# Kernel tuning notes

Hardware: AMD Instinct MI355X
Metric: run time of the kernel (lower is better)

The kernel has to match this reference:

```python
import jax, jax.numpy as jnp
import numpy as np

H = 16          # num_heads
D = 1024        # in_features
NH = D // H     # per-head dim
EPS = 1e-5


def _ln(x, g, b):
    m = jnp.mean(x, axis=-1, keepdims=True)
    v = jnp.mean((x - m) ** 2, axis=-1, keepdims=True)
    return (x - m) / jnp.sqrt(v + EPS) * g + b


def _mha(q, k, v, Wq, bq, Wk, bk, Wv, bv, causal):
    # q: [Tq,B,D], k/v: [Tk,B,D]
    Tq, B, _ = q.shape
    Tk = k.shape[0]
    qh = (q @ Wq + bq).reshape(Tq, B, H, NH)
    kh = (k @ Wk + bk).reshape(Tk, B, H, NH)
    vh = (v @ Wv + bv).reshape(Tk, B, H, NH)
    scale = 1.0 / np.float32(np.sqrt(NH))
    logits = jnp.einsum('qbhd,kbhd->bhqk', qh, kh) * scale  # [B,H,Tq,Tk]
    if causal:
        mask = jnp.tril(jnp.ones((Tq, Tk), dtype=bool))
        logits = jnp.where(mask, logits, -jnp.inf)  # softmax over prefix [0..t]
    w = jax.nn.softmax(logits, axis=-1)
    out = jnp.einsum('bhqk,kbhd->qbhd', w, vh).reshape(Tq, B, D)
    return out


def setup_inputs() -> dict:
    key = jax.random.key(0)
    ks = jax.random.split(key, 12)
    s = 0.02
    T, B = 1024, 8
    inp = {
        'encoder_input': jax.random.normal(ks[0], (T, B, D), jnp.float32),
        'decoder_input': jax.random.normal(ks[1], (T, B, D), jnp.float32),
        # self-attention projections
        'Wq1': jax.random.normal(ks[2], (D, D), jnp.float32) * s,
        'bq1': jnp.zeros((D,), jnp.float32),
        'Wk1': jax.random.normal(ks[3], (D, D), jnp.float32) * s,
        'bk1': jnp.zeros((D,), jnp.float32),
        'Wv1': jax.random.normal(ks[4], (D, D), jnp.float32) * s,
        'bv1': jnp.zeros((D,), jnp.float32),
        # cross-attention projections
        'Wq2': jax.random.normal(ks[5], (D, D), jnp.float32) * s,
        'bq2': jnp.zeros((D,), jnp.float32),
        'Wk2': jax.random.normal(ks[6], (D, D), jnp.float32) * s,
        'bk2': jnp.zeros((D,), jnp.float32),
        'Wv2': jax.random.normal(ks[7], (D, D), jnp.float32) * s,
        'bv2': jnp.zeros((D,), jnp.float32),
        # position-wise linear
        'Wl': jax.random.normal(ks[8], (D, D), jnp.float32) * s,
        'bl': jnp.zeros((D,), jnp.float32),
        # layernorms
        'g1': jnp.ones((D,), jnp.float32), 'be1': jnp.zeros((D,), jnp.float32),
        'g2': jnp.ones((D,), jnp.float32), 'be2': jnp.zeros((D,), jnp.float32),
        'g3': jnp.ones((D,), jnp.float32), 'be3': jnp.zeros((D,), jnp.float32),
    }
    return inp


def reference(encoder_input, decoder_input,
              Wq1, bq1, Wk1, bk1, Wv1, bv1,
              Wq2, bq2, Wk2, bk2, Wv2, bv2,
              Wl, bl, g1, be1, g2, be2, g3, be3):
    # causal self-attention (prefix [:t+1] per step == causal mask)
    x = _mha(decoder_input, decoder_input, decoder_input,
             Wq1, bq1, Wk1, bk1, Wv1, bv1, causal=True)
    x = _ln(x + decoder_input, g1, be1)
    # cross-attention over full encoder input
    y = _mha(x, encoder_input, encoder_input,
             Wq2, bq2, Wk2, bk2, Wv2, bv2, causal=False)
    y = _ln(y + x, g2, be2)
    # position-wise linear (no activation in source) + residual + LN
    z = y @ Wl + bl
    out = _ln(z + y, g3, be3)
    return out
```

## Files before the change

### kernel.cpp

```cpp
#include <hip/hip_runtime.h>
#include <hip/hip_bf16.h>

typedef __bf16 bf16x8 __attribute__((ext_vector_type(8)));
typedef float f32x4 __attribute__((ext_vector_type(4)));

#define MFMA16(A, B, C) __builtin_amdgcn_mfma_f32_16x16x32_bf16(A, B, C, 0, 0, 0)

#define GLDS(gp, lp)                                                              \
    __builtin_amdgcn_global_load_lds(                                             \
        (const __attribute__((address_space(1))) void*)(gp),                      \
        (__attribute__((address_space(3))) void*)(lp), 16, 0, 0)

struct PtrW { const float* p[7]; };
__global__ __launch_bounds__(256) void wt_transpose(PtrW W, __hip_bfloat16* __restrict__ Wt) {
    const float* __restrict__ src = W.p[blockIdx.z];
    __hip_bfloat16* __restrict__ dst = Wt + ((size_t)blockIdx.z << 20);
    __shared__ float tile[32][33];
    const int bn = blockIdx.x * 32;
    const int bk = blockIdx.y * 32;
    const int tx = threadIdx.x, ty = threadIdx.y;
#pragma unroll
    for (int i = 0; i < 4; i++) {
        tile[ty + i * 8][tx] = src[(size_t)(bk + ty + i * 8) * 1024 + bn + tx];
    }
    __syncthreads();
#pragma unroll
    for (int i = 0; i < 4; i++) {
        dst[(size_t)(bn + ty + i * 8) * 1024 + bk + tx] =
            __float2bfloat16(tile[tx][ty + i * 8]);
    }
}

struct PtrC { const float* s[2]; __hip_bfloat16* d[2]; };
__global__ __launch_bounds__(256) void to_bf16(PtrC c) {
    const int z = blockIdx.y;
    const int i = (blockIdx.x * 256 + threadIdx.x) * 4;
    const float4 v = *(const float4*)(c.s[z] + i);
    __align__(8) __hip_bfloat16 t[4] = {__float2bfloat16(v.x), __float2bfloat16(v.y),
                                        __float2bfloat16(v.z), __float2bfloat16(v.w)};
    *(uint2*)(c.d[z] + i) = *(const uint2*)t;
}

struct Ptr2 { const float* p[2]; };
__global__ __launch_bounds__(256) void bias_concat(Ptr2 srcs, float* __restrict__ dst) {
    const int i = threadIdx.x * 4;
    *(float4*)(dst + blockIdx.x * 1024 + i) = *(const float4*)(srcs.p[blockIdx.x] + i);
}

__global__ __launch_bounds__(256) void gemm_bias_kernel(
    const __hip_bfloat16* __restrict__ A, const __hip_bfloat16* __restrict__ Bt,
    const float* __restrict__ bias, float* __restrict__ Cf,
    __hip_bfloat16* __restrict__ Cb, int M, int N, int K,
    float qscale, int qcols) {
    __shared__ __align__(16) __hip_bfloat16 As[2][128 * 32];
    __shared__ __align__(16) __hip_bfloat16 Bs[2][128 * 32];
    const int tid = threadIdx.x;
    const int wave = tid >> 6, lane = tid & 63;
    const int quad = lane >> 4, l16 = lane & 15;
    const int m0 = blockIdx.x * 128, n0 = blockIdx.y * 128;
    const int wm = (wave & 1) * 64, wn = (wave >> 1) * 64;
    const int srow = lane >> 2;
    const int lc = (lane & 3) ^ ((lane >> 3) & 3);
    const __hip_bfloat16* ap[2];
    const __hip_bfloat16* bp[2];
    int loff[2];
#pragma unroll
    for (int u = 0; u < 2; u++) {
        const int g = wave * 2 + u;
        const int row = g * 16 + srow;
        ap[u] = A + (size_t)(m0 + row) * K + lc * 8;
        bp[u] = Bt + (size_t)(n0 + row) * K + lc * 8;
        loff[u] = g * 512;
    }
    const int pch = quad ^ ((l16 >> 1) & 3);
    f32x4 acc[4][4] = {};
#pragma unroll
    for (int u = 0; u < 2; u++) {
        GLDS(ap[u], &As[0][loff[u]]);
        GLDS(bp[u], &Bs[0][loff[u]]);
    }
    int sel = 0;
    for (int k0 = 0; k0 < K; k0 += 32) {
        __syncthreads();
        if (k0 + 32 < K) {
#pragma unroll
            for (int u = 0; u < 2; u++) {
                GLDS(ap[u] + k0 + 32, &As[sel ^ 1][loff[u]]);
                GLDS(bp[u] + k0 + 32, &Bs[sel ^ 1][loff[u]]);
            }
        }
        bf16x8 af[4], bfr[4];
#pragma unroll
        for (int i = 0; i < 4; i++) {
            af[i] = *(const bf16x8*)(&As[sel][(wm + i * 16 + l16) * 32 + pch * 8]);
            bfr[i] = *(const bf16x8*)(&Bs[sel][(wn + i * 16 + l16) * 32 + pch * 8]);
        }
#pragma unroll
        for (int i = 0; i < 4; i++)
#pragma unroll
            for (int j = 0; j < 4; j++)
                acc[i][j] = MFMA16(af[i], bfr[j], acc[i][j]);
        sel ^= 1;
    }
#pragma unroll
    for (int i = 0; i < 4; i++) {
#pragma unroll
        for (int j = 0; j < 4; j++) {
            const int mr = m0 + wm + i * 16 + quad * 4;
            const int nc = n0 + wn + j * 16 + l16;
            const float sc = (nc < qcols) ? qscale : 1.0f;
            const float bv = bias[nc];
#pragma unroll
            for (int r = 0; r < 4; r++) {
                const float v = (acc[i][j][r] + bv) * sc;
                const size_t idx = (size_t)(mr + r) * N + nc;
                if (Cf) Cf[idx] = v;
                if (Cb) Cb[idx] = __float2bfloat16(v);
            }
        }
    }
}

__global__ __launch_bounds__(256) void gemm_vt_kernel(
    const __hip_bfloat16* __restrict__ A, const __hip_bfloat16* __restrict__ X,
    const float* __restrict__ bias, __hip_bfloat16* __restrict__ Vt) {
    __shared__ __align__(16) __hip_bfloat16 As[2][128 * 32];
    __shared__ __align__(16) __hip_bfloat16 Bs[2][128 * 32];
    const int tid = threadIdx.x;
    const int wave = tid >> 6, lane = tid & 63;
    const int quad = lane >> 4, l16 = lane & 15;
    const int m0 = blockIdx.x * 128, n0 = blockIdx.y * 128;
    const int bb = blockIdx.z;
    const int wm = (wave & 1) * 64, wn = (wave >> 1) * 64;
    const int srow = lane >> 2;
    const int lc = (lane & 3) ^ ((lane >> 3) & 3);
    const __hip_bfloat16* ap[2];
    const __hip_bfloat16* bp[2];
    int loff[2];
#pragma unroll
    for (int u = 0; u < 2; u++) {
        const int g = wave * 2 + u;
        const int row = g * 16 + srow;
        ap[u] = A + (size_t)(m0 + row) * 1024 + lc * 8;
        bp[u] = X + ((size_t)(n0 + row) * 8 + bb) * 1024 + lc * 8;
        loff[u] = g * 512;
    }
    const int pch = quad ^ ((l16 >> 1) & 3);
    f32x4 acc[4][4] = {};
#pragma unroll
    for (int u = 0; u < 2; u++) {
        GLDS(ap[u], &As[0][loff[u]]);
        GLDS(bp[u], &Bs[0][loff[u]]);
    }
    int sel = 0;
    for (int k0 = 0; k0 < 1024; k0 += 32) {
        __syncthreads();
        if (k0 + 32 < 1024) {
#pragma unroll
            for (int u = 0; u < 2; u++) {
                GLDS(ap[u] + k0 + 32, &As[sel ^ 1][loff[u]]);
                GLDS(bp[u] + k0 + 32, &Bs[sel ^ 1][loff[u]]);
            }
        }
        bf16x8 af[4], bfr[4];
#pragma unroll
        for (int i = 0; i < 4; i++) {
            af[i] = *(const bf16x8*)(&As[sel][(wm + i * 16 + l16) * 32 + pch * 8]);
            bfr[i] = *(const bf16x8*)(&Bs[sel][(wn + i * 16 + l16) * 32 + pch * 8]);
        }
#pragma unroll
        for (int i = 0; i < 4; i++)
#pragma unroll
            for (int j = 0; j < 4; j++)
                acc[i][j] = MFMA16(af[i], bfr[j], acc[i][j]);
        sel ^= 1;
    }
#pragma unroll
    for (int i = 0; i < 4; i++) {
        const int mr = m0 + wm + i * 16 + quad * 4;
        float bias_r[4];
#pragma unroll
        for (int r = 0; r < 4; r++) bias_r[r] = bias[mr + r];
#pragma unroll
        for (int j = 0; j < 4; j++) {
            const int nc = n0 + wn + j * 16 + l16;
#pragma unroll
            for (int r = 0; r < 4; r++) {
                const int d = mr + r;
                const size_t idx = ((size_t)bb << 20) + ((size_t)(d >> 6) << 16) +
                                   (size_t)(d & 63) * 1024 + nc;
                Vt[idx] = __float2bfloat16(acc[i][j][r] + bias_r[r]);
            }
        }
    }
}

__global__ __launch_bounds__(256) void attn_kernel(
    const __hip_bfloat16* __restrict__ Qp, const __hip_bfloat16* __restrict__ Kp,
    const __hip_bfloat16* __restrict__ Vt, __hip_bfloat16* __restrict__ Ob,
    int T, int qRS, int kRS, int causal) {
    __shared__ __align__(16) __hip_bfloat16 Ks[2][64 * 64];
    __shared__ __align__(16) __hip_bfloat16 Vs[2][64 * 64];
    __shared__ __align__(16) __hip_bfloat16 Ps[4][16 * 64];
    const int tid = threadIdx.x, wave = tid >> 6, lane = tid & 63;
    const int quad = lane >> 4, l16 = lane & 15;
    const int gid = blockIdx.x;
    const int bh = (gid & 7) * 16 + ((gid >> 3) & 15);
    const int qt = 7 - (gid >> 7);
    const int b = bh & 7, h = bh >> 3;
    const int q0 = qt * 128;
    const int qstride = 8 * qRS, kstride = 8 * kRS;
    const int sw = l16 & 7;

    const int qg0 = q0 + wave * 16;
    const int qg1 = qg0 + 64;
    const int myq0 = qg0 + l16, myq1 = qg1 + l16;
    const __hip_bfloat16* qbase = Qp + (size_t)b * qRS + h * 64;
    const bf16x8 qf00 = *(const bf16x8*)(qbase + (size_t)myq0 * qstride + quad * 8);
    const bf16x8 qf01 = *(const bf16x8*)(qbase + (size_t)myq0 * qstride + 32 + quad * 8);
    const bf16x8 qf10 = *(const bf16x8*)(qbase + (size_t)myq1 * qstride + quad * 8);
    const bf16x8 qf11 = *(const bf16x8*)(qbase + (size_t)myq1 * qstride + 32 + quad * 8);
    bf16x8 onesf;
#pragma unroll
    for (int i = 0; i < 8; i++) onesf[i] = (__bf16)1.0f;

    const int jk = wave * 2;
    const int lrow = lane >> 3;
    const int lch = (lane & 7) ^ (lrow & 7);
    const __hip_bfloat16* kp0 =
        Kp + (size_t)b * kRS + h * 64 + (size_t)(jk * 8 + lrow) * kstride + lch * 8;
    const __hip_bfloat16* kp1 = kp0 + (size_t)8 * kstride;
    const __hip_bfloat16* vp0 =
        Vt + ((size_t)(b * 16 + h) << 16) + (size_t)(jk * 8 + lrow) * 1024 + lch * 8;
    const __hip_bfloat16* vp1 = vp0 + 8 * 1024;
    const size_t kinc = (size_t)64 * kstride;

    f32x4 o0[4] = {}, o1[4] = {};
    f32x4 ol0 = {}, ol1 = {};
    bf16x8 pf00, pf01, pf10, pf11;

    auto softmax = [&](f32x4* s, f32x4& ol, bf16x8& pf0, bf16x8& pf1, int qg, int myq,
                       int k0) {
        const bool nm = causal && (k0 + 63 > qg);
        if (nm) {
#pragma unroll
            for (int n = 0; n < 4; n++)
#pragma unroll
                for (int r = 0; r < 4; r++)
                    if (k0 + n * 16 + quad * 4 + r > myq) s[n][r] = -1e30f;
        }
#pragma unroll
        for (int n = 0; n < 4; n++) {
            const float p0 = __builtin_amdgcn_exp2f(s[n][0]);
            const float p1 = __builtin_amdgcn_exp2f(s[n][1]);
            const float p2 = __builtin_amdgcn_exp2f(s[n][2]);
            const float p3 = __builtin_amdgcn_exp2f(s[n][3]);
            const __hip_bfloat162 pa = __float22bfloat162_rn(make_float2(p0, p1));
            const __hip_bfloat162 pb = __float22bfloat162_rn(make_float2(p2, p3));
            uint2 w;
            w.x = *(const unsigned int*)&pa;
            w.y = *(const unsigned int*)&pb;
            const int gcp = 2 * n + (quad >> 1);
            *(uint2*)(&Ps[wave][l16 * 64 + ((gcp ^ sw) << 3) + (quad & 1) * 4]) = w;
        }
        pf0 = *(const bf16x8*)(&Ps[wave][l16 * 64 + ((quad ^ sw) << 3)]);
        pf1 = *(const bf16x8*)(&Ps[wave][l16 * 64 + (((quad + 4) ^ sw) << 3)]);
        ol = MFMA16(onesf, pf0, ol);
        ol = MFMA16(onesf, pf1, ol);
    };

    const int kend = causal ? (q0 + 128) : T;
    GLDS(kp0, &Ks[0][jk * 512]);
    GLDS(kp1, &Ks[0][jk * 512 + 512]);
    GLDS(vp0, &Vs[0][jk * 512]);
    GLDS(vp1, &Vs[0][jk * 512 + 512]);
    const __hip_bfloat16* kn0 = kp0 + kinc;
    const __hip_bfloat16* kn1 = kp1 + kinc;
    const __hip_bfloat16* vn0 = vp0 + 64;
    const __hip_bfloat16* vn1 = vp1 + 64;
    int sel = 0;
    for (int k0 = 0; k0 < kend; k0 += 64) {
        __syncthreads();
        if (k0 + 64 < kend) {
            GLDS(kn0, &Ks[sel ^ 1][jk * 512]);
            GLDS(kn1, &Ks[sel ^ 1][jk * 512 + 512]);
            GLDS(vn0, &Vs[sel ^ 1][jk * 512]);
            GLDS(vn1, &Vs[sel ^ 1][jk * 512 + 512]);
            kn0 += kinc; kn1 += kinc; vn0 += 64; vn1 += 64;
        }
        const bool act0 = !causal || (k0 <= qg0 + 15);
        f32x4 s0[4] = {}, s1[4] = {};
        {
            bf16x8 kf[4];
#pragma unroll
            for (int n = 0; n < 4; n++)
                kf[n] = *(const bf16x8*)(&Ks[sel][(n * 16 + l16) * 64 +
                                                  ((quad ^ sw) << 3)]);
#pragma unroll
            for (int n = 0; n < 4; n++) {
                if (act0) s0[n] = MFMA16(kf[n], qf00, s0[n]);
                s1[n] = MFMA16(kf[n], qf10, s1[n]);
            }
#pragma unroll
            for (int n = 0; n < 4; n++)
                kf[n] = *(const bf16x8*)(&Ks[sel][(n * 16 + l16) * 64 +
                                                  (((quad + 4) ^ sw) << 3)]);
#pragma unroll
            for (int n = 0; n < 4; n++) {
                if (act0) s0[n] = MFMA16(kf[n], qf01, s0[n]);
                s1[n] = MFMA16(kf[n], qf11, s1[n]);
            }
        }
        if (act0) softmax(s0, ol0, pf00, pf01, qg0, myq0, k0);
        softmax(s1, ol1, pf10, pf11, qg1, myq1, k0);
#pragma unroll
        for (int mm = 0; mm < 4; mm++) {
            const int vrow = (mm * 16 + l16) * 64;
            const bf16x8 vf0 = *(const bf16x8*)(&Vs[sel][vrow + ((quad ^ sw) << 3)]);
            const bf16x8 vf1 = *(const bf16x8*)(&Vs[sel][vrow + (((quad + 4) ^ sw) << 3)]);
            if (act0) {
                o0[mm] = MFMA16(vf0, pf00, o0[mm]);
                o0[mm] = MFMA16(vf1, pf01, o0[mm]);
            }
            o1[mm] = MFMA16(vf0, pf10, o1[mm]);
            o1[mm] = MFMA16(vf1, pf11, o1[mm]);
        }
        sel ^= 1;
    }
    const float inv0 = 1.0f / ol0[0];
    const float inv1 = 1.0f / ol1[0];
    __hip_bfloat16* ob0 = Ob + (size_t)b * 1024 + h * 64 + (size_t)myq0 * 8192;
    __hip_bfloat16* ob1 = Ob + (size_t)b * 1024 + h * 64 + (size_t)myq1 * 8192;
#pragma unroll
    for (int mm = 0; mm < 4; mm++) {
        __align__(8) __hip_bfloat16 t0[4] = {
            __float2bfloat16(o0[mm][0] * inv0), __float2bfloat16(o0[mm][1] * inv0),
            __float2bfloat16(o0[mm][2] * inv0), __float2bfloat16(o0[mm][3] * inv0)};
        *(uint2*)(ob0 + mm * 16 + quad * 4) = *(const uint2*)t0;
        __align__(8) __hip_bfloat16 t1[4] = {
            __float2bfloat16(o1[mm][0] * inv1), __float2bfloat16(o1[mm][1] * inv1),
            __float2bfloat16(o1[mm][2] * inv1), __float2bfloat16(o1[mm][3] * inv1)};
        *(uint2*)(ob1 + mm * 16 + quad * 4) = *(const uint2*)t1;
    }
}

__global__ __launch_bounds__(256) void ln_res_kernel(
    const __hip_bfloat16* __restrict__ a, const float* __restrict__ resf,
    const __hip_bfloat16* __restrict__ resb, const float* __restrict__ g,
    const float* __restrict__ be, float* __restrict__ outf,
    __hip_bfloat16* __restrict__ outb) {
    const int tid = threadIdx.x, wave = tid >> 6, lane = tid & 63;
    const int row = blockIdx.x * 4 + wave;
    const size_t base = (size_t)row * 1024;
    float x[16];
#pragma unroll
    for (int c = 0; c < 4; c++) {
        const int off = c * 256 + lane * 4;
        const uint2 ar = *(const uint2*)(a + base + off);
        const __hip_bfloat16* ah = (const __hip_bfloat16*)&ar;
        if (resf) {
            const float4 rv = *(const float4*)(resf + base + off);
            x[c * 4 + 0] = __bfloat162float(ah[0]) + rv.x;
            x[c * 4 + 1] = __bfloat162float(ah[1]) + rv.y;
            x[c * 4 + 2] = __bfloat162float(ah[2]) + rv.z;
            x[c * 4 + 3] = __bfloat162float(ah[3]) + rv.w;
        } else {
            const uint2 br = *(const uint2*)(resb + base + off);
            const __hip_bfloat16* bhp = (const __hip_bfloat16*)&br;
#pragma unroll
            for (int k = 0; k < 4; k++)
                x[c * 4 + k] = __bfloat162float(ah[k]) + __bfloat162float(bhp[k]);
        }
    }
    float s = 0.f, ss = 0.f;
#pragma unroll
    for (int k = 0; k < 16; k++) {
        s += x[k];
        ss += x[k] * x[k];
    }
#pragma unroll
    for (int w = 32; w >= 1; w >>= 1) {
        s += __shfl_xor(s, w);
        ss += __shfl_xor(ss, w);
    }
    const float mean = s * (1.f / 1024.f);
    const float inv = rsqrtf(ss * (1.f / 1024.f) - mean * mean + 1e-5f);
#pragma unroll
    for (int c = 0; c < 4; c++) {
        const int off = c * 256 + lane * 4;
        const float4 gg = *(const float4*)(g + off);
        const float4 bb = *(const float4*)(be + off);
        float y[4];
        y[0] = (x[c * 4 + 0] - mean) * inv * gg.x + bb.x;
        y[1] = (x[c * 4 + 1] - mean) * inv * gg.y + bb.y;
        y[2] = (x[c * 4 + 2] - mean) * inv * gg.z + bb.z;
        y[3] = (x[c * 4 + 3] - mean) * inv * gg.w + bb.w;
        if (outf) *(float4*)(outf + base + off) = make_float4(y[0], y[1], y[2], y[3]);
        if (outb) {
            __align__(8) __hip_bfloat16 t[4] = {
                __float2bfloat16(y[0]), __float2bfloat16(y[1]),
                __float2bfloat16(y[2]), __float2bfloat16(y[3])};
            *(uint2*)(outb + base + off) = *(const uint2*)t;
        }
    }
}

extern "C" void kernel_launch(void* const* d_in, const int* in_sizes, int n_in,
                              void* d_out, int out_size, void* d_ws, size_t ws_size,
                              hipStream_t stream) {
    const float* enc = (const float*)d_in[0];
    const float* dec = (const float*)d_in[1];
    const float* Wq1 = (const float*)d_in[2];
    const float* bq1 = (const float*)d_in[3];
    const float* Wk1 = (const float*)d_in[4];
    const float* bk1 = (const float*)d_in[5];
    const float* Wv1 = (const float*)d_in[6];
    const float* bv1 = (const float*)d_in[7];
    const float* Wq2 = (const float*)d_in[8];
    const float* bq2 = (const float*)d_in[9];
    const float* Wk2 = (const float*)d_in[10];
    const float* bk2 = (const float*)d_in[11];
    const float* Wv2 = (const float*)d_in[12];
    const float* bv2 = (const float*)d_in[13];
    const float* Wl = (const float*)d_in[14];
    const float* bl = (const float*)d_in[15];
    const float* g1 = (const float*)d_in[16];
    const float* be1 = (const float*)d_in[17];
    const float* g2 = (const float*)d_in[18];
    const float* be2 = (const float*)d_in[19];
    const float* g3 = (const float*)d_in[20];
    const float* be3 = (const float*)d_in[21];
    float* outp = (float*)d_out;

    char* p = (char*)d_ws;
    auto alloc = [&](size_t n) {
        char* r = p;
        p += (n + 255) & ~(size_t)255;
        return r;
    };
    const size_t MD = (size_t)8192 * 1024;
    __hip_bfloat16* enc_b = (__hip_bfloat16*)alloc(MD * 2);
    __hip_bfloat16* dec_b = (__hip_bfloat16*)alloc(MD * 2);
    __hip_bfloat16* Wt = (__hip_bfloat16*)alloc((size_t)7 * 1024 * 1024 * 2);
    float* bcat = (float*)alloc(2048 * sizeof(float));
    __hip_bfloat16* qk = (__hip_bfloat16*)alloc(MD * 2 * 2);
    __hip_bfloat16* qb = (__hip_bfloat16*)alloc(MD * 2);
    __hip_bfloat16* attnb = (__hip_bfloat16*)alloc(MD * 2);
    __hip_bfloat16* Vtb = (__hip_bfloat16*)alloc(MD * 2);
    __hip_bfloat16* xb = dec_b;
    __hip_bfloat16* yb = enc_b;

    const float QSC = 0.18033688f;

    PtrW wptrs = {{Wq1, Wk1, Wv1, Wq2, Wk2, Wv2, Wl}};
    wt_transpose<<<dim3(32, 32, 7), dim3(32, 8), 0, stream>>>(wptrs, Wt);
    PtrC cp = {{enc, dec}, {enc_b, dec_b}};
    to_bf16<<<dim3(8192, 2), 256, 0, stream>>>(cp);
    Ptr2 bp = {{bq1, bk1}};
    bias_concat<<<2, 256, 0, stream>>>(bp, bcat);

    gemm_bias_kernel<<<dim3(64, 16), 256, 0, stream>>>(dec_b, Wt, bcat, nullptr, qk,
                                                       8192, 2048, 1024, QSC, 1024);
    gemm_vt_kernel<<<dim3(8, 8, 8), 256, 0, stream>>>(Wt + (size_t)2 * 1024 * 1024,
                                                      dec_b, bv1, Vtb);
    attn_kernel<<<1024, 256, 0, stream>>>(qk, qk + 1024, Vtb, attnb,
                                          1024, 2048, 2048, 1);
    ln_res_kernel<<<2048, 256, 0, stream>>>(attnb, dec, nullptr, g1, be1, nullptr, xb);

    gemm_bias_kernel<<<dim3(64, 8), 256, 0, stream>>>(
        xb, Wt + (size_t)3 * 1024 * 1024, bq2, nullptr, qb, 8192, 1024, 1024, QSC, 1024);
    gemm_bias_kernel<<<dim3(64, 8), 256, 0, stream>>>(
        enc_b, Wt + (size_t)4 * 1024 * 1024, bk2, nullptr, qk, 8192, 1024, 1024, 1.0f, 0);
    gemm_vt_kernel<<<dim3(8, 8, 8), 256, 0, stream>>>(Wt + (size_t)5 * 1024 * 1024,
                                                      enc_b, bv2, Vtb);
    attn_kernel<<<1024, 256, 0, stream>>>(qb, qk, Vtb, attnb, 1024, 1024, 1024, 0);
    ln_res_kernel<<<2048, 256, 0, stream>>>(attnb, nullptr, xb, g2, be2, nullptr, yb);

    gemm_bias_kernel<<<dim3(64, 8), 256, 0, stream>>>(
        yb, Wt + (size_t)6 * 1024 * 1024, bl, nullptr, qb, 8192, 1024, 1024, 1.0f, 0);
    ln_res_kernel<<<2048, 256, 0, stream>>>(qb, nullptr, yb, g3, be3, outp, nullptr);
}
```

Baseline: 514.6 us.

## Batch independent projection GEMMs into one grouped multi-job launch

Merges the self-attention QK/V projections and the encoder-side cross-attention K/V projections into a single grouped GEMM launch of 2560 blocks. This removes launch gaps and tail underutilisation between small GEMMs. It also hoists the encoder K/V work ahead of the first attention, which needs extra workspace buffers for K2 and V2. Separately, the attention block order flips so causal query tiles run in ascending rather than descending order, which may hurt load balance for the causal pass.

```diff
diff --git a/kernel.cpp b/kernel.cpp
--- a/kernel.cpp
+++ b/kernel.cpp
@@ -47,20 +47,48 @@
     *(float4*)(dst + blockIdx.x * 1024 + i) = *(const float4*)(srcs.p[blockIdx.x] + i);
 }
 
-__global__ __launch_bounds__(256) void gemm_bias_kernel(
-    const __hip_bfloat16* __restrict__ A, const __hip_bfloat16* __restrict__ Bt,
-    const float* __restrict__ bias, float* __restrict__ Cf,
-    __hip_bfloat16* __restrict__ Cb, int M, int N, int K,
-    float qscale, int qcols) {
+struct Job {
+    const __hip_bfloat16* A;
+    const __hip_bfloat16* B;
+    const float* bias;
+    __hip_bfloat16* out;
+    int bstride;
+    int N;
+    int nblocks;
+    int gx;
+    float qscale;
+    int qcols;
+};
+struct Jobs { Job j[4]; int njobs; };
+
+__global__ __launch_bounds__(256) void gemm_multi(Jobs J) {
+    int bid = blockIdx.x;
+    int ji = 0;
+    while (ji < J.njobs - 1 && bid >= J.j[ji].nblocks) {
+        bid -= J.j[ji].nblocks;
+        ji++;
+    }
+    const Job job = J.j[ji];
+    int bx, by, bb;
+    if (job.N) {
+        bx = bid % job.gx;
+        by = bid / job.gx;
+        bb = 0;
+    } else {
+        bx = bid & 7;
+        by = (bid >> 3) & 7;
+        bb = bid >> 6;
+    }
     __shared__ __align__(16) __hip_bfloat16 As[2][128 * 32];
     __shared__ __align__(16) __hip_bfloat16 Bs[2][128 * 32];
     const int tid = threadIdx.x;
     const int wave = tid >> 6, lane = tid & 63;
     const int quad = lane >> 4, l16 = lane & 15;
-    const int m0 = blockIdx.x * 128, n0 = blockIdx.y * 128;
+    const int m0 = bx * 128, n0 = by * 128;
     const int wm = (wave & 1) * 64, wn = (wave >> 1) * 64;
     const int srow = lane >> 2;
     const int lc = (lane & 3) ^ ((lane >> 3) & 3);
+    const __hip_bfloat16* Bbase = job.B + (job.N ? 0 : bb * 1024);
     const __hip_bfloat16* ap[2];
     const __hip_bfloat16* bp[2];
     int loff[2];
@@ -68,81 +96,8 @@
     for (int u = 0; u < 2; u++) {
         const int g = wave * 2 + u;
         const int row = g * 16 + srow;
-        ap[u] = A + (size_t)(m0 + row) * K + lc * 8;
-        bp[u] = Bt + (size_t)(n0 + row) * K + lc * 8;
-        loff[u] = g * 512;
-    }
-    const int pch = quad ^ ((l16 >> 1) & 3);
-    f32x4 acc[4][4] = {};
-#pragma unroll
-    for (int u = 0; u < 2; u++) {
-        GLDS(ap[u], &As[0][loff[u]]);
-        GLDS(bp[u], &Bs[0][loff[u]]);
-    }
-    int sel = 0;
-    for (int k0 = 0; k0 < K; k0 += 32) {
-        __syncthreads();
-        if (k0 + 32 < K) {
-#pragma unroll
-            for (int u = 0; u < 2; u++) {
-                GLDS(ap[u] + k0 + 32, &As[sel ^ 1][loff[u]]);
-                GLDS(bp[u] + k0 + 32, &Bs[sel ^ 1][loff[u]]);
-            }
-        }
-        bf16x8 af[4], bfr[4];
-#pragma unroll
-        for (int i = 0; i < 4; i++) {
-            af[i] = *(const bf16x8*)(&As[sel][(wm + i * 16 + l16) * 32 + pch * 8]);
-            bfr[i] = *(const bf16x8*)(&Bs[sel][(wn + i * 16 + l16) * 32 + pch * 8]);
-        }
-#pragma unroll
-        for (int i = 0; i < 4; i++)
-#pragma unroll
-            for (int j = 0; j < 4; j++)
-                acc[i][j] = MFMA16(af[i], bfr[j], acc[i][j]);
-        sel ^= 1;
-    }
-#pragma unroll
-    for (int i = 0; i < 4; i++) {
-#pragma unroll
-        for (int j = 0; j < 4; j++) {
-            const int mr = m0 + wm + i * 16 + quad * 4;
-            const int nc = n0 + wn + j * 16 + l16;
-            const float sc = (nc < qcols) ? qscale : 1.0f;
-            const float bv = bias[nc];
-#pragma unroll
-            for (int r = 0; r < 4; r++) {
-                const float v = (acc[i][j][r] + bv) * sc;
-                const size_t idx = (size_t)(mr + r) * N + nc;
-                if (Cf) Cf[idx] = v;
-                if (Cb) Cb[idx] = __float2bfloat16(v);
-            }
-        }
-    }
-}
-
-__global__ __launch_bounds__(256) void gemm_vt_kernel(
-    const __hip_bfloat16* __restrict__ A, const __hip_bfloat16* __restrict__ X,
-    const float* __restrict__ bias, __hip_bfloat16* __restrict__ Vt) {
-    __shared__ __align__(16) __hip_bfloat16 As[2][128 * 32];
-    __shared__ __align__(16) __hip_bfloat16 Bs[2][128 * 32];
-    const int tid = threadIdx.x;
-    const int wave = tid >> 6, lane = tid & 63;
-    const int quad = lane >> 4, l16 = lane & 15;
-    const int m0 = blockIdx.x * 128, n0 = blockIdx.y * 128;
-    const int bb = blockIdx.z;
-    const int wm = (wave & 1) * 64, wn = (wave >> 1) * 64;
-    const int srow = lane >> 2;
-    const int lc = (lane & 3) ^ ((lane >> 3) & 3);
-    const __hip_bfloat16* ap[2];
-    const __hip_bfloat16* bp[2];
-    int loff[2];
-#pragma unroll
-    for (int u = 0; u < 2; u++) {
-        const int g = wave * 2 + u;
-        const int row = g * 16 + srow;
-        ap[u] = A + (size_t)(m0 + row) * 1024 + lc * 8;
-        bp[u] = X + ((size_t)(n0 + row) * 8 + bb) * 1024 + lc * 8;
+        ap[u] = job.A + (size_t)(m0 + row) * 1024 + lc * 8;
+        bp[u] = Bbase + (size_t)(n0 + row) * job.bstride + lc * 8;
         loff[u] = g * 512;
     }
     const int pch = quad ^ ((l16 >> 1) & 3);
@@ -175,21 +130,39 @@
                 acc[i][j] = MFMA16(af[i], bfr[j], acc[i][j]);
         sel ^= 1;
     }
-#pragma unroll
-    for (int i = 0; i < 4; i++) {
-        const int mr = m0 + wm + i * 16 + quad * 4;
-        float bias_r[4];
-#pragma unroll
-        for (int r = 0; r < 4; r++) bias_r[r] = bias[mr + r];
-#pragma unroll
-        for (int j = 0; j < 4; j++) {
-            const int nc = n0 + wn + j * 16 + l16;
-#pragma unroll
-            for (int r = 0; r < 4; r++) {
-                const int d = mr + r;
-                const size_t idx = ((size_t)bb << 20) + ((size_t)(d >> 6) << 16) +
-                                   (size_t)(d & 63) * 1024 + nc;
-                Vt[idx] = __float2bfloat16(acc[i][j][r] + bias_r[r]);
+    if (job.N) {
+#pragma unroll
+        for (int i = 0; i < 4; i++) {
+#pragma unroll
+            for (int j = 0; j < 4; j++) {
+                const int mr = m0 + wm + i * 16 + quad * 4;
+                const int nc = n0 + wn + j * 16 + l16;
+                const float sc = (nc < job.qcols) ? job.qscale : 1.0f;
+                const float bv = job.bias[nc];
+#pragma unroll
+                for (int r = 0; r < 4; r++) {
+                    const float v = (acc[i][j][r] + bv) * sc;
+                    job.out[(size_t)(mr + r) * job.N + nc] = __float2bfloat16(v);
+                }
+            }
+        }
+    } else {
+#pragma unroll
+        for (int i = 0; i < 4; i++) {
+            const int mr = m0 + wm + i * 16 + quad * 4;
+            float bias_r[4];
+#pragma unroll
+            for (int r = 0; r < 4; r++) bias_r[r] = job.bias[mr + r];
+#pragma unroll
+            for (int j = 0; j < 4; j++) {
+                const int nc = n0 + wn + j * 16 + l16;
+#pragma unroll
+                for (int r = 0; r < 4; r++) {
+                    const int d = mr + r;
+                    const size_t idx = ((size_t)bb << 20) + ((size_t)(d >> 6) << 16) +
+                                       (size_t)(d & 63) * 1024 + nc;
+                    job.out[idx] = __float2bfloat16(acc[i][j][r] + bias_r[r]);
+                }
             }
         }
     }
@@ -206,7 +179,7 @@
     const int quad = lane >> 4, l16 = lane & 15;
     const int gid = blockIdx.x;
     const int bh = (gid & 7) * 16 + ((gid >> 3) & 15);
-    const int qt = 7 - (gid >> 7);
+    const int qt = gid >> 7;
     const int b = bh & 7, h = bh >> 3;
     const int q0 = qt * 128;
     const int qstride = 8 * qRS, kstride = 8 * kRS;
@@ -444,9 +417,11 @@
     __hip_bfloat16* Wt = (__hip_bfloat16*)alloc((size_t)7 * 1024 * 1024 * 2);
     float* bcat = (float*)alloc(2048 * sizeof(float));
     __hip_bfloat16* qk = (__hip_bfloat16*)alloc(MD * 2 * 2);
+    __hip_bfloat16* k2b = (__hip_bfloat16*)alloc(MD * 2);
     __hip_bfloat16* qb = (__hip_bfloat16*)alloc(MD * 2);
     __hip_bfloat16* attnb = (__hip_bfloat16*)alloc(MD * 2);
     __hip_bfloat16* Vtb = (__hip_bfloat16*)alloc(MD * 2);
+    __hip_bfloat16* Vtb2 = (__hip_bfloat16*)alloc(MD * 2);
     __hip_bfloat16* xb = dec_b;
     __hip_bfloat16* yb = enc_b;
 
@@ -459,24 +434,34 @@
     Ptr2 bp = {{bq1, bk1}};
     bias_concat<<<2, 256, 0, stream>>>(bp, bcat);
 
-    gemm_bias_kernel<<<dim3(64, 16), 256, 0, stream>>>(dec_b, Wt, bcat, nullptr, qk,
-                                                       8192, 2048, 1024, QSC, 1024);
-    gemm_vt_kernel<<<dim3(8, 8, 8), 256, 0, stream>>>(Wt + (size_t)2 * 1024 * 1024,
-                                                      dec_b, bv1, Vtb);
+    {
+        Jobs J;
+        J.j[0] = {dec_b, Wt, bcat, qk, 1024, 2048, 64 * 16, 64, QSC, 1024};
+        J.j[1] = {Wt + ((size_t)2 << 20), dec_b, bv1, Vtb, 8192, 0, 512, 8, 1.0f, 0};
+        J.j[2] = {enc_b, Wt + ((size_t)4 << 20), bk2, k2b, 1024, 1024, 64 * 8, 64, 1.0f, 0};
+        J.j[3] = {Wt + ((size_t)5 << 20), enc_b, bv2, Vtb2, 8192, 0, 512, 8, 1.0f, 0};
+        J.njobs = 4;
+        gemm_multi<<<2560, 256, 0, stream>>>(J);
+    }
+
     attn_kernel<<<1024, 256, 0, stream>>>(qk, qk + 1024, Vtb, attnb,
                                           1024, 2048, 2048, 1);
     ln_res_kernel<<<2048, 256, 0, stream>>>(attnb, dec, nullptr, g1, be1, nullptr, xb);
 
-    gemm_bias_kernel<<<dim3(64, 8), 256, 0, stream>>>(
-        xb, Wt + (size_t)3 * 1024 * 1024, bq2, nullptr, qb, 8192, 1024, 1024, QSC, 1024);
-    gemm_bias_kernel<<<dim3(64, 8), 256, 0, stream>>>(
-        enc_b, Wt + (size_t)4 * 1024 * 1024, bk2, nullptr, qk, 8192, 1024, 1024, 1.0f, 0);
-    gemm_vt_kernel<<<dim3(8, 8, 8), 256, 0, stream>>>(Wt + (size_t)5 * 1024 * 1024,
-                                                      enc_b, bv2, Vtb);
-    attn_kernel<<<1024, 256, 0, stream>>>(qb, qk, Vtb, attnb, 1024, 1024, 1024, 0);
+    {
+        Jobs J;
+        J.j[0] = {xb, Wt + ((size_t)3 << 20), bq2, qb, 1024, 1024, 64 * 8, 64, QSC, 1024};
+        J.njobs = 1;
+        gemm_multi<<<512, 256, 0, stream>>>(J);
+    }
+    attn_kernel<<<1024, 256, 0, stream>>>(qb, k2b, Vtb2, attnb, 1024, 1024, 1024, 0);
     ln_res_kernel<<<2048, 256, 0, stream>>>(attnb, nullptr, xb, g2, be2, nullptr, yb);
 
-    gemm_bias_kernel<<<dim3(64, 8), 256, 0, stream>>>(
-        yb, Wt + (size_t)6 * 1024 * 1024, bl, nullptr, qb, 8192, 1024, 1024, 1.0f, 0);
+    {
+        Jobs J;
+        J.j[0] = {yb, Wt + ((size_t)6 << 20), bl, qb, 1024, 1024, 64 * 8, 64, 1.0f, 0};
+        J.njobs = 1;
+        gemm_multi<<<512, 256, 0, stream>>>(J);
+    }
     ln_res_kernel<<<2048, 256, 0, stream>>>(qb, nullptr, yb, g3, be3, outp, nullptr);
 }
```

Result: no change. 524.2 us (+1.9%).
